# Optimization experiments

Hardware: AMD Instinct MI355X
Metric: run time of the kernel (lower is better)

The kernel has to match this reference:

```python
import math
import jax, jax.numpy as jnp
import numpy as np

D = 1152      # vision_dim
P = 14        # patch
IMG = 896     # image_size
CIN = 3       # vision_channels
L = 2         # vision_blocks
MLP = 4304    # vision_mlp_hidden
EPS = 1e-6
B = 1
N = (IMG // P) ** 2  # 4096 tokens


def _ln(x, w, b):
    m = jnp.mean(x, axis=-1, keepdims=True)
    v = jnp.mean(jnp.square(x - m), axis=-1, keepdims=True)
    return (x - m) * jax.lax.rsqrt(v + EPS) * w + b


def setup_inputs() -> dict:
    key = jax.random.key(0)
    ks = jax.random.split(key, 20)
    s = 0.02
    inp = {
        "img": jax.random.normal(ks[0], (B, CIN, IMG, IMG), jnp.float32),
        "patch_w": jax.random.normal(ks[1], (D, CIN, P, P), jnp.float32) * s,
        "patch_b": jnp.zeros((D,), jnp.float32),
        "pos": jax.random.normal(ks[2], (D, N), jnp.float32) * s,
        # per-block params stacked along leading L axis (torch Linear: [out, in])
        "ln1_w": jnp.ones((L, D), jnp.float32),
        "ln1_b": jnp.zeros((L, D), jnp.float32),
        "qkv_w": jax.random.normal(ks[3], (L, 3 * D, D), jnp.float32) * s,
        "qkv_b": jnp.zeros((L, 3 * D), jnp.float32),
        "proj_w": jax.random.normal(ks[4], (L, D, D), jnp.float32) * s,
        "proj_b": jnp.zeros((L, D), jnp.float32),
        "ln2_w": jnp.ones((L, D), jnp.float32),
        "ln2_b": jnp.zeros((L, D), jnp.float32),
        "fc1_w": jax.random.normal(ks[5], (L, MLP, D), jnp.float32) * s,
        "fc1_b": jnp.zeros((L, MLP), jnp.float32),
        "fc2_w": jax.random.normal(ks[6], (L, D, MLP), jnp.float32) * s,
        "fc2_b": jnp.zeros((L, D), jnp.float32),
        "post_w": jnp.ones((D,), jnp.float32),
        "post_b": jnp.zeros((D,), jnp.float32),
    }
    return inp


def reference(img, patch_w, patch_b, pos, ln1_w, ln1_b, qkv_w, qkv_b,
              proj_w, proj_b, ln2_w, ln2_b, fc1_w, fc1_b, fc2_w, fc2_b,
              post_w, post_b):
    # conv patch embed (kernel=stride=P, valid padding)
    x = jax.lax.conv_general_dilated(
        img, patch_w, window_strides=(P, P), padding="VALID",
        dimension_numbers=("NCHW", "OIHW", "NCHW"))
    x = x + patch_b[None, :, None, None]
    x = x.reshape(B, D, N).transpose(0, 2, 1)          # [B, N, D]
    x = x + pos.T[None, :, :]

    scale = 1.0 / math.sqrt(D)

    def blk(x, p):
        l1w, l1b, qw, qb, pw, pb, l2w, l2b, f1w, f1b, f2w, f2b = p
        h = _ln(x, l1w, l1b)
        qkv = jnp.einsum("bnd,ed->bne", h, qw) + qb     # [B, N, 3D]
        q, k, v = jnp.split(qkv, 3, axis=-1)            # single-head, full D
        attn = jax.nn.softmax(jnp.einsum("bnd,bmd->bnm", q, k) * scale, axis=-1)
        y = jnp.einsum("bnm,bmd->bnd", attn, v)
        x = x + jnp.einsum("bnd,ed->bne", y, pw) + pb
        h = _ln(x, l2w, l2b)
        h = jax.nn.gelu(jnp.einsum("bnd,md->bnm", h, f1w) + f1b, approximate=False)
        x = x + jnp.einsum("bnm,dm->bnd", h, f2w) + f2b
        return x, None

    x, _ = jax.lax.scan(blk, x, (ln1_w, ln1_b, qkv_w, qkv_b, proj_w, proj_b,
                                 ln2_w, ln2_b, fc1_w, fc1_b, fc2_w, fc2_b))
    return _ln(x, post_w, post_b)
```

## Files before the change

### kernel.cpp

```cpp
#include <hip/hip_runtime.h>

#define NT 4096
#define DD 1152
#define D3 3456
#define D3P 3584
#define MLP_R 4304
#define MLP_P 4352
#define KP 640

typedef unsigned short u16;
typedef short v8s __attribute__((ext_vector_type(8)));
typedef float v4f __attribute__((ext_vector_type(4)));

__device__ __forceinline__ u16 f2b(float f) {
    unsigned int u = __builtin_bit_cast(unsigned int, f);
    u += 0x7fffu + ((u >> 16) & 1u);
    return (u16)(u >> 16);
}
__device__ __forceinline__ float b2f(u16 s) {
    unsigned int u = ((unsigned int)s) << 16;
    return __builtin_bit_cast(float, u);
}

__device__ __forceinline__ void async16(const void* g, void* l) {
    __builtin_amdgcn_global_load_lds(
        (const __attribute__((address_space(1))) void*)g,
        (__attribute__((address_space(3))) void*)l, 16, 0, 0);
}

__device__ __forceinline__ unsigned lds_off(const void* p) {
    return (unsigned)(size_t)(const __attribute__((address_space(3))) void*)p;
}
__device__ __forceinline__ v8s ldsr(unsigned byte_off) {
    v8s r;
    asm volatile("ds_read_b128 %0, %1" : "=v"(r) : "v"(byte_off));
    return r;
}

__device__ __forceinline__ float gelu_f(float t) {
    float u = t * (0.7978845608028654f + 0.03567740814183026f * t * t);
    return t / (1.0f + __expf(-2.0f * u));
}

template<int EPI>
__global__ __launch_bounds__(512, 4)
void gemm2p(const u16* __restrict__ A, const u16* __restrict__ B, int ld,
            int Kdim, const float* __restrict__ bias,
            const float* __restrict__ aux, float* __restrict__ outf,
            u16* __restrict__ outb, int ldc, int NNT)
{
    __shared__ __align__(128) union { u16 kl[2][16384]; float sc[8][64][17]; } sm;
    const int tid  = threadIdx.x, lane = tid & 63, wave = tid >> 6;
    const int wr   = wave >> 2, wc = wave & 3;
    const int fr   = lane & 15, kqh = lane >> 4;

    const int nwg  = gridDim.x;
    const int bidx = (int)blockIdx.x;
    const int wg   = (bidx & 7) * (nwg >> 3) + (bidx >> 3);
    const int mt   = wg / NNT, nt = wg % NNT;
    const int bm0  = mt * 128, bn0 = nt * 128;

    const int c    = tid;
    const int s_lr = (c >> 7) * 16 + ((c >> 2) & 15);
    const int s_lc = ((((c >> 6) & 1) * 4) + ((c & 3) ^ (((c >> 5) & 1) << 1))) * 8;
    const size_t s_off = (size_t)s_lr * ld + s_lc;
    const unsigned koff2 = (unsigned)(fr * 64 + ((kqh * 16) ^ ((fr & 8) << 2)));

    u16* kb = sm.kl[0];
    const unsigned lbase = lds_off(kb);

    auto stage = [&](int bi, int reg, const u16* gRowBase) {
        u16* lb = kb + bi * 16384 + reg * 4096;
        async16(gRowBase + s_off, lb + tid * 8);
        async16(gRowBase + s_off + (size_t)64 * ld, lb + (512 + tid) * 8);
    };
    auto srcA = [&](int t) { return A + (size_t)bm0 * ld + t * 64; };
    auto srcB = [&](int t) { return B + (size_t)bn0 * ld + t * 64; };

    v4f acc[4][2];
    const v4f vzero = {0.f, 0.f, 0.f, 0.f};
#pragma unroll
    for (int i = 0; i < 4; ++i) { acc[i][0] = vzero; acc[i][1] = vzero; }

    const int NKT = Kdim >> 6;

    stage(0, 0, srcA(0));
    stage(0, 2, srcB(0));
    if (NKT > 1) {
        stage(1, 2, srcB(1));
        asm volatile("s_waitcnt vmcnt(2)" ::: "memory");
    } else {
        asm volatile("s_waitcnt vmcnt(0)" ::: "memory");
    }
    __builtin_amdgcn_s_barrier();

    v8s a[8], b0f[2], b1f[2];
    for (int t = 0; t < NKT; ++t) {
        const int bi = t & 1;
        const unsigned AB = lbase + bi * 32768;
        const unsigned BB = AB + 16384;

#pragma unroll
        for (int mi = 0; mi < 4; ++mi)
#pragma unroll
            for (int ks = 0; ks < 2; ++ks)
                a[mi * 2 + ks] = ldsr(AB + ((wr * 4 + mi) * 2 + ks) * 1024 + koff2);
#pragma unroll
        for (int ks = 0; ks < 2; ++ks)
            b0f[ks] = ldsr(BB + ((wc * 2 + 0) * 2 + ks) * 1024 + koff2);
#pragma unroll
        for (int ks = 0; ks < 2; ++ks)
            b1f[ks] = ldsr(BB + ((wc * 2 + 1) * 2 + ks) * 1024 + koff2);
        if (t + 1 < NKT) stage(bi ^ 1, 0, srcA(t + 1));
        __builtin_amdgcn_s_barrier();
        asm volatile("s_waitcnt lgkmcnt(0)" ::: "memory");
        __builtin_amdgcn_sched_barrier(0);
        __builtin_amdgcn_s_setprio(1);
#pragma unroll
        for (int mi = 0; mi < 4; ++mi)
#pragma unroll
            for (int ks = 0; ks < 2; ++ks)
                acc[mi][0] = __builtin_amdgcn_mfma_f32_16x16x32_bf16(
                    a[mi * 2 + ks], b0f[ks], acc[mi][0], 0, 0, 0);
        __builtin_amdgcn_s_setprio(0);
        __builtin_amdgcn_s_barrier();

        if (t + 2 < NKT) stage(bi, 2, srcB(t + 2));
        __builtin_amdgcn_s_setprio(1);
#pragma unroll
        for (int mi = 0; mi < 4; ++mi)
#pragma unroll
            for (int ks = 0; ks < 2; ++ks)
                acc[mi][1] = __builtin_amdgcn_mfma_f32_16x16x32_bf16(
                    a[mi * 2 + ks], b1f[ks], acc[mi][1], 0, 0, 0);
        __builtin_amdgcn_s_setprio(0);
        if (t + 2 < NKT) { asm volatile("s_waitcnt vmcnt(2)" ::: "memory"); }
        else             { asm volatile("s_waitcnt vmcnt(0)" ::: "memory"); }
        __builtin_amdgcn_s_barrier();
    }

    const int cn = lane & 15;
    const int cm = (lane >> 4) * 4;
    float (*S)[17] = sm.sc[wave];
    const int gm = bm0 + wr * 64 + lane;
#pragma unroll
    for (int jp = 0; jp < 2; ++jp) {
        __syncthreads();
#pragma unroll
        for (int i = 0; i < 4; ++i)
#pragma unroll
            for (int r = 0; r < 4; ++r)
                S[i * 16 + cm + r][cn] = acc[i][jp][r];
        __syncthreads();
        const int gn0 = bn0 + wc * 32 + jp * 16;
        float v[16];
#pragma unroll
        for (int cc = 0; cc < 16; ++cc) v[cc] = S[lane][cc];
        if constexpr (EPI <= 2) {
            union { u16 us[16]; uint4 q4[2]; } o;
#pragma unroll
            for (int cc = 0; cc < 16; ++cc) {
                float tv = v[cc];
                if constexpr (EPI >= 1) tv += bias[gn0 + cc];
                if constexpr (EPI == 2) tv = gelu_f(tv);
                o.us[cc] = f2b(tv);
            }
            uint4* dst = (uint4*)(outb + (size_t)gm * ldc + gn0);
            dst[0] = o.q4[0];
            dst[1] = o.q4[1];
        } else {
            float* dst = outf + (size_t)gm * ldc + gn0;
            const float* ax = aux + (size_t)gm * ldc + gn0;
#pragma unroll
            for (int cc = 0; cc < 4; ++cc) {
                float4 a4 = ((const float4*)ax)[cc];
                float4 r4;
                r4.x = a4.x + v[4 * cc + 0] + bias[gn0 + 4 * cc + 0];
                r4.y = a4.y + v[4 * cc + 1] + bias[gn0 + 4 * cc + 1];
                r4.z = a4.z + v[4 * cc + 2] + bias[gn0 + 4 * cc + 2];
                r4.w = a4.w + v[4 * cc + 3] + bias[gn0 + 4 * cc + 3];
                ((float4*)dst)[cc] = r4;
            }
        }
    }
}

template<int EPI>
__global__ __launch_bounds__(512, 2)
void gemm8p(const u16* __restrict__ A, const u16* __restrict__ B, int ld,
            int Kdim, const float* __restrict__ bias,
            u16* __restrict__ outb, int ldc, int NNT, u16* __restrict__ vt)
{
    __shared__ __align__(128) union { u16 kl[2][32768]; u16 ep[8][8192]; } sm;
    const int tid  = threadIdx.x, lane = tid & 63, wave = tid >> 6;
    const int wr   = wave >> 2, wc = wave & 3;
    const int fr   = lane & 15, kqh = lane >> 4;

    const int nwg  = gridDim.x;
    const int bidx = (int)blockIdx.x;
    const int wg   = (bidx & 7) * (nwg >> 3) + (bidx >> 3);
    const int mt   = wg / NNT, nt = wg % NNT;
    const int bm0  = mt * 256, bn0 = nt * 256;

    const int c    = tid;
    const int s_lr = (c >> 7) * 16 + ((c >> 2) & 15);
    const int s_lc = ((((c >> 6) & 1) * 4) + ((c & 3) ^ (((c >> 5) & 1) << 1))) * 8;
    const size_t s_off = (size_t)s_lr * ld + s_lc;
    const unsigned koff2 = (unsigned)(fr * 64 + ((kqh * 16) ^ ((fr & 8) << 2)));

    u16* kb = sm.kl[0];
    const unsigned lbase = lds_off(kb);

    auto stage = [&](int bi, int reg, const u16* gRowBase) {
        u16* lb = kb + bi * 32768 + reg * 4096;
        async16(gRowBase + s_off, lb + tid * 8);
        async16(gRowBase + s_off + (size_t)64 * ld, lb + (512 + tid) * 8);
    };
    auto srcA = [&](int h, int t) { return A + (size_t)(bm0 + h * 128) * ld + t * 64; };
    auto srcB = [&](int h, int t) { return B + (size_t)(bn0 + h * 128) * ld + t * 64; };

    v4f acc[8][4];
    const v4f vzero = {0.f, 0.f, 0.f, 0.f};
#pragma unroll
    for (int i = 0; i < 8; ++i)
#pragma unroll
        for (int j = 0; j < 4; ++j) acc[i][j] = vzero;

    const int NKT = Kdim >> 6;

    stage(0, 4, srcB(0, 0));
    stage(0, 6, srcB(1, 0));
    stage(0, 0, srcA(0, 0));
    stage(0, 2, srcA(1, 0));
    if (NKT > 1) {
        stage(1, 4, srcB(0, 1));
        stage(1, 6, srcB(1, 1));
        asm volatile("s_waitcnt vmcnt(4)" ::: "memory");
    } else {
        asm volatile("s_waitcnt vmcnt(0)" ::: "memory");
    }
    __builtin_amdgcn_s_barrier();

    v8s a[8], b0f[4], b1f[4];
    for (int t = 0; t < NKT; ++t) {
        const int bi = t & 1;
        const unsigned AB = lbase + bi * 65536 + wr * 16384;
        const unsigned BB = lbase + bi * 65536 + 32768 + (wc >> 1) * 16384;
        const unsigned bs = (wc & 1) * 8192;

#pragma unroll
        for (int mi = 0; mi < 4; ++mi)
#pragma unroll
            for (int ks = 0; ks < 2; ++ks)
                a[mi * 2 + ks] = ldsr(AB + (mi * 2 + ks) * 1024 + koff2);
#pragma unroll
        for (int nj = 0; nj < 2; ++nj)
#pragma unroll
            for (int ks = 0; ks < 2; ++ks)
                b0f[nj * 2 + ks] = ldsr(BB + bs + (nj * 2 + ks) * 1024 + koff2);
        if (t + 1 < NKT) stage(bi ^ 1, 0, srcA(0, t + 1));
        __builtin_amdgcn_s_barrier();
        asm volatile("s_waitcnt lgkmcnt(0)" ::: "memory");
        __builtin_amdgcn_sched_barrier(0);
        __builtin_amdgcn_s_setprio(1);
#pragma unroll
        for (int mi = 0; mi < 4; ++mi)
#pragma unroll
            for (int nj = 0; nj < 2; ++nj)
#pragma unroll
                for (int ks = 0; ks < 2; ++ks)
                    acc[mi][nj] = __builtin_amdgcn_mfma_f32_16x16x32_bf16(
                        a[mi * 2 + ks], b0f[nj * 2 + ks], acc[mi][nj], 0, 0, 0);
        __builtin_amdgcn_s_setprio(0);
        __builtin_amdgcn_s_barrier();

#pragma unroll
        for (int nj = 0; nj < 2; ++nj)
#pragma unroll
            for (int ks = 0; ks < 2; ++ks)
                b1f[nj * 2 + ks] = ldsr(BB + bs + (4 + nj * 2 + ks) * 1024 + koff2);
        if (t + 1 < NKT) stage(bi ^ 1, 2, srcA(1, t + 1));
        __builtin_amdgcn_s_barrier();
        asm volatile("s_waitcnt lgkmcnt(0)" ::: "memory");
        __builtin_amdgcn_sched_barrier(0);
        __builtin_amdgcn_s_setprio(1);
#pragma unroll
        for (int mi = 0; mi < 4; ++mi)
#pragma unroll
            for (int nj = 0; nj < 2; ++nj)
#pragma unroll
                for (int ks = 0; ks < 2; ++ks)
                    acc[mi][2 + nj] = __builtin_amdgcn_mfma_f32_16x16x32_bf16(
                        a[mi * 2 + ks], b1f[nj * 2 + ks], acc[mi][2 + nj], 0, 0, 0);
        __builtin_amdgcn_s_setprio(0);
        __builtin_amdgcn_s_barrier();

#pragma unroll
        for (int mi = 0; mi < 4; ++mi)
#pragma unroll
            for (int ks = 0; ks < 2; ++ks)
                a[mi * 2 + ks] = ldsr(AB + (8 + mi * 2 + ks) * 1024 + koff2);
        if (t + 2 < NKT) stage(bi, 4, srcB(0, t + 2));
        __builtin_amdgcn_s_barrier();
        asm volatile("s_waitcnt lgkmcnt(0)" ::: "memory");
        __builtin_amdgcn_sched_barrier(0);
        __builtin_amdgcn_s_setprio(1);
#pragma unroll
        for (int mi = 0; mi < 4; ++mi)
#pragma unroll
            for (int nj = 0; nj < 2; ++nj)
#pragma unroll
                for (int ks = 0; ks < 2; ++ks)
                    acc[4 + mi][2 + nj] = __builtin_amdgcn_mfma_f32_16x16x32_bf16(
                        a[mi * 2 + ks], b1f[nj * 2 + ks], acc[4 + mi][2 + nj], 0, 0, 0);
        __builtin_amdgcn_s_setprio(0);
        __builtin_amdgcn_s_barrier();

        if (t + 2 < NKT) stage(bi, 6, srcB(1, t + 2));
        __builtin_amdgcn_s_barrier();
        __builtin_amdgcn_s_setprio(1);
#pragma unroll
        for (int mi = 0; mi < 4; ++mi)
#pragma unroll
            for (int nj = 0; nj < 2; ++nj)
#pragma unroll
                for (int ks = 0; ks < 2; ++ks)
                    acc[4 + mi][nj] = __builtin_amdgcn_mfma_f32_16x16x32_bf16(
                        a[mi * 2 + ks], b0f[nj * 2 + ks], acc[4 + mi][nj], 0, 0, 0);
        __builtin_amdgcn_s_setprio(0);
        if (t + 2 < NKT) { asm volatile("s_waitcnt vmcnt(4)" ::: "memory"); }
        else             { asm volatile("s_waitcnt vmcnt(0)" ::: "memory"); }
        __builtin_amdgcn_s_barrier();
    }

    asm volatile("s_waitcnt vmcnt(0)" ::: "memory");
    __builtin_amdgcn_s_barrier();
    u16* ew = sm.ep[wave];
    float bcol[4];
    if constexpr (EPI >= 1) {
#pragma unroll
        for (int nj = 0; nj < 4; ++nj)
            bcol[nj] = bias[bn0 + wc * 64 + nj * 16 + fr];
    }
#pragma unroll
    for (int mi = 0; mi < 8; ++mi)
#pragma unroll
        for (int nj = 0; nj < 4; ++nj)
#pragma unroll
            for (int r = 0; r < 4; ++r) {
                int row = mi * 16 + kqh * 4 + r;
                int ec  = nj * 16 + fr;
                float t = acc[mi][nj][r];
                if constexpr (EPI >= 1) t += bcol[nj];
                if constexpr (EPI == 2) t = gelu_f(t);
                ew[row * 64 + (ec ^ (((row >> 2) & 3) << 4))] = f2b(t);
            }
    __syncthreads();
    const int gc = bn0 + wc * 64 + (lane & 7) * 8;
    const bool inV = (EPI == 1) && (vt != nullptr) && gc >= 2304 && gc < D3;
#pragma unroll
    for (int p = 0; p < 16; ++p) {
        int row = p * 8 + (lane >> 3);
        int key = (row >> 2) & 3;
        v8s ch = *(const v8s*)(ew + row * 64 + (((lane & 7) * 8) ^ (key << 4)));
        size_t gm = (size_t)(bm0 + wr * 128 + row);
        *(uint4*)(outb + gm * ldc + gc) = __builtin_bit_cast(uint4, ch);
        if constexpr (EPI == 1) {
            if (inV) {
                union { v8s v; u16 us[8]; } cu; cu.v = ch;
#pragma unroll
                for (int j = 0; j < 8; ++j)
                    vt[(size_t)(gc + j - 2304) * NT + gm] = cu.us[j];
            }
        }
    }
}

template<int EPI, int MT, int DBUF = 0>
__global__ __launch_bounds__(256)
void gemm_bt(const u16* __restrict__ A, int lda,
             const u16* __restrict__ B, int ldb, int Kdim,
             const float* __restrict__ bias, const float* __restrict__ aux,
             float* __restrict__ outf, u16* __restrict__ outb, int ldc,
             u16* __restrict__ vt, int NX)
{
    constexpr int JT = (MT == 128) ? 4 : 2;
    constexpr int AR = MT * 8 / 256;
    constexpr int NB = DBUF ? 2 : 1;

    __shared__ union SM {
        struct { u16 a[NB * MT * 64]; u16 b[NB * 128 * 64]; } st;
        float sc[4][64][17];
    } sm;

    const int b    = blockIdx.x;
    const int MY   = (gridDim.x >> 3) / NX;
    const int q    = b >> 3;
    const int m0   = ((b & 7) * MY + q % MY) * MT;
    const int n0   = (q / MY) * 128;

    const int tid  = threadIdx.x;
    const int lane = tid & 63;
    const int wave = tid >> 6;
    const int wm   = (MT == 128) ? (wave & 1) * 64 : 0;
    const int wn   = (MT == 128) ? (wave >> 1) * 64 : wave * 32;
    const int fr   = lane & 15;
    const int kqh  = lane >> 4;
    const int swz  = fr & 7;

    v4f acc[4][JT];
    const v4f vzero = {0.f, 0.f, 0.f, 0.f};
#pragma unroll
    for (int i = 0; i < 4; ++i)
#pragma unroll
        for (int j = 0; j < JT; ++j) acc[i][j] = vzero;

    auto stage = [&](u16* As, u16* Bs, int kt) {
#pragma unroll
        for (int r = 0; r < AR; ++r) {
            int c = r * 256 + tid;
            int row = c >> 3;
            int kc = (c & 7) ^ (row & 7);
            async16(A + (size_t)(m0 + row) * lda + kt + kc * 8, As + c * 8);
        }
#pragma unroll
        for (int r = 0; r < 4; ++r) {
            int c = r * 256 + tid;
            int row = c >> 3;
            int kc = (c & 7) ^ (row & 7);
            async16(B + (size_t)(n0 + row) * ldb + kt + kc * 8, Bs + c * 8);
        }
    };

    auto compute = [&](const u16* As, const u16* Bs) {
#pragma unroll
        for (int ks = 0; ks < 2; ++ks) {
            const int kq = ks * 4 + kqh;
            const int kp = (kq ^ swz) * 8;
            v8s af[4], bf[JT];
#pragma unroll
            for (int i = 0; i < 4; ++i)
                af[i] = *(const v8s*)(As + (wm + i * 16 + fr) * 64 + kp);
#pragma unroll
            for (int j = 0; j < JT; ++j)
                bf[j] = *(const v8s*)(Bs + (wn + j * 16 + fr) * 64 + kp);
#pragma unroll
            for (int i = 0; i < 4; ++i)
#pragma unroll
                for (int j = 0; j < JT; ++j)
                    acc[i][j] = __builtin_amdgcn_mfma_f32_16x16x32_bf16(
                        af[i], bf[j], acc[i][j], 0, 0, 0);
        }
    };

    if constexpr (DBUF) {
        stage(sm.st.a, sm.st.b, 0);
        int cur = 0;
        for (int kt = 0; kt < Kdim; kt += 64) {
            __syncthreads();
            const int nxt = cur ^ 1;
            if (kt + 64 < Kdim)
                stage(sm.st.a + nxt * (MT * 64), sm.st.b + nxt * (128 * 64), kt + 64);
            compute(sm.st.a + cur * (MT * 64), sm.st.b + cur * (128 * 64));
            cur = nxt;
        }
    } else {
        for (int kt = 0; kt < Kdim; kt += 64) {
            stage(sm.st.a, sm.st.b, kt);
            __syncthreads();
            compute(sm.st.a, sm.st.b);
            __syncthreads();
        }
    }

    const int cn = lane & 15;
    const int cm = (lane >> 4) * 4;
    float (*S)[17] = sm.sc[wave];
    const int gm = m0 + wm + lane;
#pragma unroll
    for (int jp = 0; jp < JT; ++jp) {
        __syncthreads();
#pragma unroll
        for (int i = 0; i < 4; ++i)
#pragma unroll
            for (int r = 0; r < 4; ++r)
                S[i * 16 + cm + r][cn] = acc[i][jp][r];
        __syncthreads();
        const int gn0 = n0 + wn + jp * 16;
        float v[16];
#pragma unroll
        for (int c = 0; c < 16; ++c) v[c] = S[lane][c];
        if constexpr (EPI <= 2) {
            union { u16 us[16]; uint4 q4[2]; } o;
#pragma unroll
            for (int c = 0; c < 16; ++c) {
                float t = v[c];
                if constexpr (EPI >= 1) t += bias[gn0 + c];
                if constexpr (EPI == 2) t = gelu_f(t);
                o.us[c] = f2b(t);
            }
            uint4* dst = (uint4*)(outb + (size_t)gm * ldc + gn0);
            dst[0] = o.q4[0];
            dst[1] = o.q4[1];
            if constexpr (EPI == 1) {
                if (vt != nullptr && gn0 >= 2304) {
#pragma unroll
                    for (int c = 0; c < 16; ++c)
                        vt[(size_t)(gn0 + c - 2304) * NT + gm] = o.us[c];
                }
            }
        } else if constexpr (EPI == 3) {
            float* dst = outf + (size_t)gm * ldc + gn0;
            const float* ax = aux + (size_t)gm * ldc + gn0;
#pragma unroll
            for (int c = 0; c < 4; ++c) {
                float4 a4 = ((const float4*)ax)[c];
                float4 r4;
                r4.x = a4.x + v[4 * c + 0] + bias[gn0 + 4 * c + 0];
                r4.y = a4.y + v[4 * c + 1] + bias[gn0 + 4 * c + 1];
                r4.z = a4.z + v[4 * c + 2] + bias[gn0 + 4 * c + 2];
                r4.w = a4.w + v[4 * c + 3] + bias[gn0 + 4 * c + 3];
                ((float4*)dst)[c] = r4;
            }
        } else {
            float* dst = outf + (size_t)gm * ldc + gn0;
#pragma unroll
            for (int c = 0; c < 4; ++c) {
                float4 r4;
                r4.x = v[4 * c + 0] + bias[gn0 + 4 * c + 0] + aux[(size_t)(gn0 + 4 * c + 0) * NT + gm];
                r4.y = v[4 * c + 1] + bias[gn0 + 4 * c + 1] + aux[(size_t)(gn0 + 4 * c + 1) * NT + gm];
                r4.z = v[4 * c + 2] + bias[gn0 + 4 * c + 2] + aux[(size_t)(gn0 + 4 * c + 2) * NT + gm];
                r4.w = v[4 * c + 3] + bias[gn0 + 4 * c + 3] + aux[(size_t)(gn0 + 4 * c + 3) * NT + gm];
                ((float4*)dst)[c] = r4;
            }
        }
    }
}

template<int OUTF>
__global__ __launch_bounds__(384)
void ln_kernel(const float* __restrict__ x, const float* __restrict__ w,
               const float* __restrict__ b, void* __restrict__ out)
{
    const int n = blockIdx.x;
    const int t = threadIdx.x;
    const float* row = x + (size_t)n * DD;
    float v0 = row[t], v1 = row[t + 384], v2 = row[t + 768];
    float s  = v0 + v1 + v2;
    float ss = v0 * v0 + v1 * v1 + v2 * v2;
#pragma unroll
    for (int o = 32; o > 0; o >>= 1) {
        s  += __shfl_down(s, o);
        ss += __shfl_down(ss, o);
    }
    __shared__ float ps[6], pss[6], mh[2];
    if ((t & 63) == 0) { ps[t >> 6] = s; pss[t >> 6] = ss; }
    __syncthreads();
    if (t == 0) {
        float S = 0.f, SS = 0.f;
        for (int i = 0; i < 6; ++i) { S += ps[i]; SS += pss[i]; }
        float m = S / (float)DD;
        float var = SS / (float)DD - m * m;
        mh[0] = m;
        mh[1] = rsqrtf(var + 1e-6f);
    }
    __syncthreads();
    const float m = mh[0], rs = mh[1];
#pragma unroll
    for (int j = 0; j < 3; ++j) {
        int c = t + j * 384;
        float y = (row[c] - m) * rs * w[c] + b[c];
        if constexpr (OUTF) ((float*)out)[(size_t)n * DD + c] = y;
        else                ((u16*)out)[(size_t)n * DD + c]   = f2b(y);
    }
}

__global__ __launch_bounds__(256)
void softmax_kernel(u16* __restrict__ s)
{
    const float SC = 0.029462782549439484f;
    const int row = blockIdx.x;
    const int t = threadIdx.x;
    u16* p = s + (size_t)row * NT + t * 16;
    uint4 u0 = *(const uint4*)p;
    uint4 u1 = *(const uint4*)(p + 8);
    float v[16];
    unsigned int w[8] = {u0.x, u0.y, u0.z, u0.w, u1.x, u1.y, u1.z, u1.w};
#pragma unroll
    for (int i = 0; i < 8; ++i) {
        v[2 * i]     = b2f((u16)(w[i] & 0xffffu)) * SC;
        v[2 * i + 1] = b2f((u16)(w[i] >> 16)) * SC;
    }
    float mx = -1e30f;
#pragma unroll
    for (int i = 0; i < 16; ++i) mx = fmaxf(mx, v[i]);
#pragma unroll
    for (int o = 32; o > 0; o >>= 1) mx = fmaxf(mx, __shfl_down(mx, o));
    __shared__ float red[4];
    __shared__ float bc;
    if ((t & 63) == 0) red[t >> 6] = mx;
    __syncthreads();
    if (t == 0) bc = fmaxf(fmaxf(red[0], red[1]), fmaxf(red[2], red[3]));
    __syncthreads();
    const float M = bc;
    float sum = 0.f;
#pragma unroll
    for (int i = 0; i < 16; ++i) { v[i] = __expf(v[i] - M); sum += v[i]; }
#pragma unroll
    for (int o = 32; o > 0; o >>= 1) sum += __shfl_down(sum, o);
    __syncthreads();
    if ((t & 63) == 0) red[t >> 6] = sum;
    __syncthreads();
    if (t == 0) bc = red[0] + red[1] + red[2] + red[3];
    __syncthreads();
    const float inv = 1.0f / bc;
    union { u16 us[8]; uint4 u4; } o0, o1;
#pragma unroll
    for (int i = 0; i < 8; ++i) o0.us[i] = f2b(v[i] * inv);
#pragma unroll
    for (int i = 0; i < 8; ++i) o1.us[i] = f2b(v[8 + i] * inv);
    *(uint4*)p = o0.u4;
    *(uint4*)(p + 8) = o1.u4;
}

__global__ __launch_bounds__(256)
void im2col_kernel(const float* __restrict__ img, u16* __restrict__ a)
{
    const int k = blockIdx.x * 256 + threadIdx.x;
    const int n = blockIdx.y;
    if (k >= KP) return;
    float v = 0.f;
    if (k < 588) {
        int cin = k / 196;
        int rr = k - cin * 196;
        int py = rr / 14;
        int px = rr - py * 14;
        int gy = (n >> 6) * 14 + py;
        int gx = (n & 63) * 14 + px;
        v = img[(size_t)cin * 896 * 896 + (size_t)gy * 896 + gx];
    }
    a[(size_t)n * KP + k] = f2b(v);
}

constexpr int CV_S0 = 2 * D3P * DD / 4;
constexpr int CV_S1 = CV_S0 + 2 * DD * DD / 4;
constexpr int CV_S2 = CV_S1 + 2 * MLP_P * DD / 4;
constexpr int CV_S3 = CV_S2 + 2 * DD * MLP_P / 4;
constexpr int CV_S4 = CV_S3 + DD * KP / 4;
constexpr int CV_S5 = CV_S4 + 2 * MLP_P / 4;
constexpr int CV_S6 = CV_S5 + 2 * D3P / 4;
constexpr int CV_BLOCKS = (CV_S6 + 255) / 256;

__device__ __forceinline__ void store_bf4(u16* p, float4 f) {
    union { u16 s[4]; uint2 d; } o;
    o.s[0] = f2b(f.x); o.s[1] = f2b(f.y); o.s[2] = f2b(f.z); o.s[3] = f2b(f.w);
    *(uint2*)p = o.d;
}

__global__ __launch_bounds__(256)
void convert_all(const float* __restrict__ qkv_w, const float* __restrict__ proj_w,
                 const float* __restrict__ fc1_w, const float* __restrict__ fc2_w,
                 const float* __restrict__ patch_w, const float* __restrict__ fc1_b,
                 const float* __restrict__ qkv_b,
                 u16* __restrict__ w_qkv, u16* __restrict__ w_proj,
                 u16* __restrict__ w_fc1, u16* __restrict__ w_fc2,
                 u16* __restrict__ w_pat, float* __restrict__ fc1b_p,
                 float* __restrict__ qkvb_p)
{
    int v = blockIdx.x * 256 + threadIdx.x;
    if (v >= CV_S6) return;
    const float4 z4 = {0.f, 0.f, 0.f, 0.f};
    if (v < CV_S0) {
        size_t e = (size_t)v * 4;
        int row = (int)(e / DD);
        int c = (int)(e % DD);
        int l = row / D3P, lr = row % D3P;
        float4 f = z4;
        if (lr < D3)
            f = *(const float4*)(qkv_w + ((size_t)l * D3 + lr) * DD + c);
        store_bf4(w_qkv + e, f);
    } else if (v < CV_S1) {
        int e = v - CV_S0;
        store_bf4(w_proj + (size_t)e * 4, ((const float4*)proj_w)[e]);
    } else if (v < CV_S2) {
        size_t e = (size_t)(v - CV_S1) * 4;
        int row = (int)(e / DD);
        int c = (int)(e % DD);
        int l = row / MLP_P, lr = row % MLP_P;
        float4 f = z4;
        if (lr < MLP_R)
            f = *(const float4*)(fc1_w + ((size_t)l * MLP_R + lr) * DD + c);
        store_bf4(w_fc1 + e, f);
    } else if (v < CV_S3) {
        size_t e = (size_t)(v - CV_S2) * 4;
        int row = (int)(e / MLP_P);
        int c = (int)(e % MLP_P);
        float4 f = z4;
        if (c < MLP_R)
            f = *(const float4*)(fc2_w + (size_t)row * MLP_R + c);
        store_bf4(w_fc2 + e, f);
    } else if (v < CV_S4) {
        size_t e = (size_t)(v - CV_S3) * 4;
        int row = (int)(e / KP);
        int c = (int)(e % KP);
        float4 f = z4;
        if (c < 588)
            f = *(const float4*)(patch_w + (size_t)row * 588 + c);
        store_bf4(w_pat + e, f);
    } else if (v < CV_S5) {
        size_t e = (size_t)(v - CV_S4) * 4;
        int l = (int)(e / MLP_P);
        int c = (int)(e % MLP_P);
        float4 f = z4;
        if (c < MLP_R)
            f = *(const float4*)(fc1_b + (size_t)l * MLP_R + c);
        *(float4*)(fc1b_p + e) = f;
    } else {
        size_t e = (size_t)(v - CV_S5) * 4;
        int l = (int)(e / D3P);
        int c = (int)(e % D3P);
        float4 f = z4;
        if (c < D3)
            f = *(const float4*)(qkv_b + (size_t)l * D3 + c);
        *(float4*)(qkvb_p + e) = f;
    }
}

constexpr size_t OFF_X      = 0;
constexpr size_t OFF_HBF    = OFF_X      + (size_t)NT * DD * 4;
constexpr size_t OFF_TMP    = OFF_HBF    + (size_t)NT * DD * 2;
constexpr size_t OFF_QKV    = OFF_TMP    + (size_t)NT * MLP_P * 2;
constexpr size_t OFF_VT     = OFF_QKV    + (size_t)NT * D3P * 2;
constexpr size_t OFF_IM     = OFF_VT     + (size_t)DD * NT * 2;
constexpr size_t OFF_WQKV   = OFF_IM     + (size_t)NT * KP * 2;
constexpr size_t OFF_WPROJ  = OFF_WQKV   + (size_t)2 * D3P * DD * 2;
constexpr size_t OFF_WFC1   = OFF_WPROJ  + (size_t)2 * DD * DD * 2;
constexpr size_t OFF_WFC2   = OFF_WFC1   + (size_t)2 * MLP_P * DD * 2;
constexpr size_t OFF_WPATCH = OFF_WFC2   + (size_t)2 * DD * MLP_P * 2;
constexpr size_t OFF_FC1B   = OFF_WPATCH + (size_t)DD * KP * 2;
constexpr size_t OFF_QKVB   = OFF_FC1B   + (size_t)2 * MLP_P * 4;

extern "C" void kernel_launch(void* const* d_in, const int* in_sizes, int n_in,
                              void* d_out, int out_size, void* d_ws, size_t ws_size,
                              hipStream_t stream)
{
    const float* img     = (const float*)d_in[0];
    const float* patch_w = (const float*)d_in[1];
    const float* patch_b = (const float*)d_in[2];
    const float* pos     = (const float*)d_in[3];
    const float* ln1_w   = (const float*)d_in[4];
    const float* ln1_b   = (const float*)d_in[5];
    const float* qkv_w   = (const float*)d_in[6];
    const float* qkv_b   = (const float*)d_in[7];
    const float* proj_w  = (const float*)d_in[8];
    const float* proj_b  = (const float*)d_in[9];
    const float* ln2_w   = (const float*)d_in[10];
    const float* ln2_b   = (const float*)d_in[11];
    const float* fc1_w   = (const float*)d_in[12];
    const float* fc1_b   = (const float*)d_in[13];
    const float* fc2_w   = (const float*)d_in[14];
    const float* fc2_b   = (const float*)d_in[15];
    const float* post_w  = (const float*)d_in[16];
    const float* post_b  = (const float*)d_in[17];

    char* ws = (char*)d_ws;
    float* x      = (float*)(ws + OFF_X);
    u16*  h_bf    = (u16*)(ws + OFF_HBF);
    u16*  tmp_bf  = (u16*)(ws + OFF_TMP);
    u16*  qkv_bf  = (u16*)(ws + OFF_QKV);
    u16*  vt      = (u16*)(ws + OFF_VT);
    u16*  a_im    = (u16*)(ws + OFF_IM);
    u16*  w_qkv   = (u16*)(ws + OFF_WQKV);
    u16*  w_proj  = (u16*)(ws + OFF_WPROJ);
    u16*  w_fc1   = (u16*)(ws + OFF_WFC1);
    u16*  w_fc2   = (u16*)(ws + OFF_WFC2);
    u16*  w_pat   = (u16*)(ws + OFF_WPATCH);
    float* fc1b_p = (float*)(ws + OFF_FC1B);
    float* qkvb_p = (float*)(ws + OFF_QKVB);

    convert_all<<<CV_BLOCKS, 256, 0, stream>>>(
        qkv_w, proj_w, fc1_w, fc2_w, patch_w, fc1_b, qkv_b,
        w_qkv, w_proj, w_fc1, w_fc2, w_pat, fc1b_p, qkvb_p);
    im2col_kernel<<<dim3(3, NT), 256, 0, stream>>>(img, a_im);

    gemm_bt<4, 64, 1><<<9 * 64, 256, 0, stream>>>(
        a_im, KP, w_pat, KP, KP, patch_b, pos, x, nullptr, DD, nullptr, 9);

    for (int l = 0; l < 2; ++l) {
        ln_kernel<0><<<NT, 384, 0, stream>>>(x, ln1_w + l * DD, ln1_b + l * DD, h_bf);
        gemm8p<1><<<224, 512, 0, stream>>>(
            h_bf, w_qkv + (size_t)l * D3P * DD, DD, DD,
            qkvb_p + (size_t)l * D3P, qkv_bf, D3P, 14, vt);
        gemm8p<0><<<256, 512, 0, stream>>>(
            qkv_bf, qkv_bf + DD, D3P, DD, nullptr, tmp_bf, NT, 16, nullptr);
        softmax_kernel<<<NT, 256, 0, stream>>>(tmp_bf);
        gemm_bt<0, 64, 1><<<9 * 64, 256, 0, stream>>>(
            tmp_bf, NT, vt, NT, NT, nullptr, nullptr, nullptr, h_bf, DD, nullptr, 9);
        gemm_bt<3, 64, 1><<<9 * 64, 256, 0, stream>>>(
            h_bf, DD, w_proj + (size_t)l * DD * DD, DD, DD,
            proj_b + (size_t)l * DD, x, x, nullptr, DD, nullptr, 9);
        ln_kernel<0><<<NT, 384, 0, stream>>>(x, ln2_w + l * DD, ln2_b + l * DD, h_bf);
        gemm2p<2><<<1088, 512, 0, stream>>>(
            h_bf, w_fc1 + (size_t)l * MLP_P * DD, DD, DD,
            fc1b_p + (size_t)l * MLP_P, nullptr, nullptr, tmp_bf, MLP_P, 34);
        gemm_bt<3, 64, 1><<<9 * 64, 256, 0, stream>>>(
            tmp_bf, MLP_P, w_fc2 + (size_t)l * DD * MLP_P, MLP_P, MLP_P,
            fc2_b + (size_t)l * DD, x, x, nullptr, DD, nullptr, 9);
    }
    ln_kernel<1><<<NT, 384, 0, stream>>>(x, post_w, post_b, d_out);
}
```

Before: 883.5 us.

## Replace gemm_bt with gemm2p for patch, PV, proj and fc2 GEMMs

Routes the four N=1152 GEMMs (patch embed, attention PV, proj and fc2) through the larger-tile 512-thread gemm2p kernel instead of the 256-thread gemm_bt kernel. To do so it adds an EPI==4 epilogue to gemm2p that reads the transposed position-embedding aux. The legacy gemm_bt kernel is removed. Larger tiles should give more data reuse per block, at the cost of only 288 workgroups, which may underfill the GPU's compute units.

```diff
diff --git a/kernel.cpp b/kernel.cpp
--- a/kernel.cpp
+++ b/kernel.cpp
@@ -168,7 +168,7 @@
             uint4* dst = (uint4*)(outb + (size_t)gm * ldc + gn0);
             dst[0] = o.q4[0];
             dst[1] = o.q4[1];
-        } else {
+        } else if constexpr (EPI == 3) {
             float* dst = outf + (size_t)gm * ldc + gn0;
             const float* ax = aux + (size_t)gm * ldc + gn0;
 #pragma unroll
@@ -179,6 +179,17 @@
                 r4.y = a4.y + v[4 * cc + 1] + bias[gn0 + 4 * cc + 1];
                 r4.z = a4.z + v[4 * cc + 2] + bias[gn0 + 4 * cc + 2];
                 r4.w = a4.w + v[4 * cc + 3] + bias[gn0 + 4 * cc + 3];
+                ((float4*)dst)[cc] = r4;
+            }
+        } else {
+            float* dst = outf + (size_t)gm * ldc + gn0;
+#pragma unroll
+            for (int cc = 0; cc < 4; ++cc) {
+                float4 r4;
+                r4.x = v[4 * cc + 0] + bias[gn0 + 4 * cc + 0] + aux[(size_t)(gn0 + 4 * cc + 0) * NT + gm];
+                r4.y = v[4 * cc + 1] + bias[gn0 + 4 * cc + 1] + aux[(size_t)(gn0 + 4 * cc + 1) * NT + gm];
+                r4.z = v[4 * cc + 2] + bias[gn0 + 4 * cc + 2] + aux[(size_t)(gn0 + 4 * cc + 2) * NT + gm];
+                r4.w = v[4 * cc + 3] + bias[gn0 + 4 * cc + 3] + aux[(size_t)(gn0 + 4 * cc + 3) * NT + gm];
                 ((float4*)dst)[cc] = r4;
             }
         }
@@ -371,167 +382,6 @@
 #pragma unroll
                 for (int j = 0; j < 8; ++j)
                     vt[(size_t)(gc + j - 2304) * NT + gm] = cu.us[j];
-            }
-        }
-    }
-}
-
-template<int EPI, int MT, int DBUF = 0>
-__global__ __launch_bounds__(256)
-void gemm_bt(const u16* __restrict__ A, int lda,
-             const u16* __restrict__ B, int ldb, int Kdim,
-             const float* __restrict__ bias, const float* __restrict__ aux,
-             float* __restrict__ outf, u16* __restrict__ outb, int ldc,
-             u16* __restrict__ vt, int NX)
-{
-    constexpr int JT = (MT == 128) ? 4 : 2;
-    constexpr int AR = MT * 8 / 256;
-    constexpr int NB = DBUF ? 2 : 1;
-
-    __shared__ union SM {
-        struct { u16 a[NB * MT * 64]; u16 b[NB * 128 * 64]; } st;
-        float sc[4][64][17];
-    } sm;
-
-    const int b    = blockIdx.x;
-    const int MY   = (gridDim.x >> 3) / NX;
-    const int q    = b >> 3;
-    const int m0   = ((b & 7) * MY + q % MY) * MT;
-    const int n0   = (q / MY) * 128;
-
-    const int tid  = threadIdx.x;
-    const int lane = tid & 63;
-    const int wave = tid >> 6;
-    const int wm   = (MT == 128) ? (wave & 1) * 64 : 0;
-    const int wn   = (MT == 128) ? (wave >> 1) * 64 : wave * 32;
-    const int fr   = lane & 15;
-    const int kqh  = lane >> 4;
-    const int swz  = fr & 7;
-
-    v4f acc[4][JT];
-    const v4f vzero = {0.f, 0.f, 0.f, 0.f};
-#pragma unroll
-    for (int i = 0; i < 4; ++i)
-#pragma unroll
-        for (int j = 0; j < JT; ++j) acc[i][j] = vzero;
-
-    auto stage = [&](u16* As, u16* Bs, int kt) {
-#pragma unroll
-        for (int r = 0; r < AR; ++r) {
-            int c = r * 256 + tid;
-            int row = c >> 3;
-            int kc = (c & 7) ^ (row & 7);
-            async16(A + (size_t)(m0 + row) * lda + kt + kc * 8, As + c * 8);
-        }
-#pragma unroll
-        for (int r = 0; r < 4; ++r) {
-            int c = r * 256 + tid;
-            int row = c >> 3;
-            int kc = (c & 7) ^ (row & 7);
-            async16(B + (size_t)(n0 + row) * ldb + kt + kc * 8, Bs + c * 8);
-        }
-    };
-
-    auto compute = [&](const u16* As, const u16* Bs) {
-#pragma unroll
-        for (int ks = 0; ks < 2; ++ks) {
-            const int kq = ks * 4 + kqh;
-            const int kp = (kq ^ swz) * 8;
-            v8s af[4], bf[JT];
-#pragma unroll
-            for (int i = 0; i < 4; ++i)
-                af[i] = *(const v8s*)(As + (wm + i * 16 + fr) * 64 + kp);
-#pragma unroll
-            for (int j = 0; j < JT; ++j)
-                bf[j] = *(const v8s*)(Bs + (wn + j * 16 + fr) * 64 + kp);
-#pragma unroll
-            for (int i = 0; i < 4; ++i)
-#pragma unroll
-                for (int j = 0; j < JT; ++j)
-                    acc[i][j] = __builtin_amdgcn_mfma_f32_16x16x32_bf16(
-                        af[i], bf[j], acc[i][j], 0, 0, 0);
-        }
-    };
-
-    if constexpr (DBUF) {
-        stage(sm.st.a, sm.st.b, 0);
-        int cur = 0;
-        for (int kt = 0; kt < Kdim; kt += 64) {
-            __syncthreads();
-            const int nxt = cur ^ 1;
-            if (kt + 64 < Kdim)
-                stage(sm.st.a + nxt * (MT * 64), sm.st.b + nxt * (128 * 64), kt + 64);
-            compute(sm.st.a + cur * (MT * 64), sm.st.b + cur * (128 * 64));
-            cur = nxt;
-        }
-    } else {
-        for (int kt = 0; kt < Kdim; kt += 64) {
-            stage(sm.st.a, sm.st.b, kt);
-            __syncthreads();
-            compute(sm.st.a, sm.st.b);
-            __syncthreads();
-        }
-    }
-
-    const int cn = lane & 15;
-    const int cm = (lane >> 4) * 4;
-    float (*S)[17] = sm.sc[wave];
-    const int gm = m0 + wm + lane;
-#pragma unroll
-    for (int jp = 0; jp < JT; ++jp) {
-        __syncthreads();
-#pragma unroll
-        for (int i = 0; i < 4; ++i)
-#pragma unroll
-            for (int r = 0; r < 4; ++r)
-                S[i * 16 + cm + r][cn] = acc[i][jp][r];
-        __syncthreads();
-        const int gn0 = n0 + wn + jp * 16;
-        float v[16];
-#pragma unroll
-        for (int c = 0; c < 16; ++c) v[c] = S[lane][c];
-        if constexpr (EPI <= 2) {
-            union { u16 us[16]; uint4 q4[2]; } o;
-#pragma unroll
-            for (int c = 0; c < 16; ++c) {
-                float t = v[c];
-                if constexpr (EPI >= 1) t += bias[gn0 + c];
-                if constexpr (EPI == 2) t = gelu_f(t);
-                o.us[c] = f2b(t);
-            }
-            uint4* dst = (uint4*)(outb + (size_t)gm * ldc + gn0);
-            dst[0] = o.q4[0];
-            dst[1] = o.q4[1];
-            if constexpr (EPI == 1) {
-                if (vt != nullptr && gn0 >= 2304) {
-#pragma unroll
-                    for (int c = 0; c < 16; ++c)
-                        vt[(size_t)(gn0 + c - 2304) * NT + gm] = o.us[c];
-                }
-            }
-        } else if constexpr (EPI == 3) {
-            float* dst = outf + (size_t)gm * ldc + gn0;
-            const float* ax = aux + (size_t)gm * ldc + gn0;
-#pragma unroll
-            for (int c = 0; c < 4; ++c) {
-                float4 a4 = ((const float4*)ax)[c];
-                float4 r4;
-                r4.x = a4.x + v[4 * c + 0] + bias[gn0 + 4 * c + 0];
-                r4.y = a4.y + v[4 * c + 1] + bias[gn0 + 4 * c + 1];
-                r4.z = a4.z + v[4 * c + 2] + bias[gn0 + 4 * c + 2];
-                r4.w = a4.w + v[4 * c + 3] + bias[gn0 + 4 * c + 3];
-                ((float4*)dst)[c] = r4;
-            }
-        } else {
-            float* dst = outf + (size_t)gm * ldc + gn0;
-#pragma unroll
-            for (int c = 0; c < 4; ++c) {
-                float4 r4;
-                r4.x = v[4 * c + 0] + bias[gn0 + 4 * c + 0] + aux[(size_t)(gn0 + 4 * c + 0) * NT + gm];
-                r4.y = v[4 * c + 1] + bias[gn0 + 4 * c + 1] + aux[(size_t)(gn0 + 4 * c + 1) * NT + gm];
-                r4.z = v[4 * c + 2] + bias[gn0 + 4 * c + 2] + aux[(size_t)(gn0 + 4 * c + 2) * NT + gm];
-                r4.w = v[4 * c + 3] + bias[gn0 + 4 * c + 3] + aux[(size_t)(gn0 + 4 * c + 3) * NT + gm];
-                ((float4*)dst)[c] = r4;
             }
         }
     }
@@ -783,8 +633,8 @@
         w_qkv, w_proj, w_fc1, w_fc2, w_pat, fc1b_p, qkvb_p);
     im2col_kernel<<<dim3(3, NT), 256, 0, stream>>>(img, a_im);
 
-    gemm_bt<4, 64, 1><<<9 * 64, 256, 0, stream>>>(
-        a_im, KP, w_pat, KP, KP, patch_b, pos, x, nullptr, DD, nullptr, 9);
+    gemm2p<4><<<288, 512, 0, stream>>>(
+        a_im, w_pat, KP, KP, patch_b, pos, x, nullptr, DD, 9);
 
     for (int l = 0; l < 2; ++l) {
         ln_kernel<0><<<NT, 384, 0, stream>>>(x, ln1_w + l * DD, ln1_b + l * DD, h_bf);
@@ -794,18 +644,18 @@
         gemm8p<0><<<256, 512, 0, stream>>>(
             qkv_bf, qkv_bf + DD, D3P, DD, nullptr, tmp_bf, NT, 16, nullptr);
         softmax_kernel<<<NT, 256, 0, stream>>>(tmp_bf);
-        gemm_bt<0, 64, 1><<<9 * 64, 256, 0, stream>>>(
-            tmp_bf, NT, vt, NT, NT, nullptr, nullptr, nullptr, h_bf, DD, nullptr, 9);
-        gemm_bt<3, 64, 1><<<9 * 64, 256, 0, stream>>>(
-            h_bf, DD, w_proj + (size_t)l * DD * DD, DD, DD,
-            proj_b + (size_t)l * DD, x, x, nullptr, DD, nullptr, 9);
+        gemm2p<0><<<288, 512, 0, stream>>>(
+            tmp_bf, vt, NT, NT, nullptr, nullptr, nullptr, h_bf, DD, 9);
+        gemm2p<3><<<288, 512, 0, stream>>>(
+            h_bf, w_proj + (size_t)l * DD * DD, DD, DD,
+            proj_b + (size_t)l * DD, x, x, nullptr, DD, 9);
         ln_kernel<0><<<NT, 384, 0, stream>>>(x, ln2_w + l * DD, ln2_b + l * DD, h_bf);
         gemm2p<2><<<1088, 512, 0, stream>>>(
             h_bf, w_fc1 + (size_t)l * MLP_P * DD, DD, DD,
             fc1b_p + (size_t)l * MLP_P, nullptr, nullptr, tmp_bf, MLP_P, 34);
-        gemm_bt<3, 64, 1><<<9 * 64, 256, 0, stream>>>(
-            tmp_bf, MLP_P, w_fc2 + (size_t)l * DD * MLP_P, MLP_P, MLP_P,
-            fc2_b + (size_t)l * DD, x, x, nullptr, DD, nullptr, 9);
+        gemm2p<3><<<288, 512, 0, stream>>>(
+            tmp_bf, w_fc2 + (size_t)l * DD * MLP_P, MLP_P, MLP_P,
+            fc2_b + (size_t)l * DD, x, x, nullptr, DD, 9);
     }
     ln_kernel<1><<<NT, 384, 0, stream>>>(x, post_w, post_b, d_out);
 }
```

Measured after the change: 924.8 us. 1.05x slower.
